# Optimization experiments

Measured on AMD Instinct MI355X. Metric: run time of the kernel, lower is better.

Reference implementation:

```python
import jax, jax.numpy as jnp
import numpy as np

TOPK = 13
NUM_CLASSES = 80
ALPHA = 1.0
BETA = 6.0
EPS = 1e-9
IOU_EPS = 1e-6  # mmdet BboxOverlaps2D union clamp


def setup_inputs() -> dict:
    key = jax.random.key(0)
    k0, k1, k2, k3, k4 = jax.random.split(key, 5)
    B, G, C = 32, 64, NUM_CLASSES
    # Prior center points for a 640x640 image, strides 8/16/32 -> 8400 priors.
    pts = []
    for s in (8, 16, 32):
        n = 640 // s
        xs = (jnp.arange(n, dtype=jnp.float32) + 0.5) * s
        gy, gx = jnp.meshgrid(xs, xs, indexing='ij')
        pts.append(jnp.stack([gx.ravel(), gy.ravel()], axis=-1))
    priors_points = jnp.concatenate(pts, axis=0)  # [8400, 2]
    P = priors_points.shape[0]
    pred_scores = jax.random.uniform(k0, (B, P, C), dtype=jnp.float32)
    half = jax.random.uniform(k1, (B, P, 2), minval=8.0, maxval=64.0)
    pred_bboxes = jnp.concatenate([priors_points[None] - half,
                                   priors_points[None] + half], axis=-1)
    xy = jax.random.uniform(k2, (B, G, 2), minval=0.0, maxval=560.0)
    wh = jax.random.uniform(k3, (B, G, 2), minval=16.0, maxval=80.0)
    gt_bboxes = jnp.concatenate([xy, xy + wh], axis=-1)
    gt_labels = jax.random.randint(k4, (B, G, 1), 0, C).astype(jnp.int64)
    pad_bbox_flag = jnp.ones((B, G, 1), jnp.float32)
    return {
        'pred_scores': pred_scores,
        'pred_bboxes': pred_bboxes,
        'priors_points': priors_points,
        'gt_labels': gt_labels,
        'gt_bboxes': gt_bboxes,
        'pad_bbox_flag': pad_bbox_flag,
    }


def _pairwise_iou(gt_bboxes, pred_bboxes):
    # gt [B,G,4], pred [B,P,4] (xyxy) -> IoU [B,G,P]
    lt = jnp.maximum(gt_bboxes[:, :, None, :2], pred_bboxes[:, None, :, :2])
    rb = jnp.minimum(gt_bboxes[:, :, None, 2:], pred_bboxes[:, None, :, 2:])
    wh = jnp.clip(rb - lt, 0.0)
    inter = wh[..., 0] * wh[..., 1]
    area_g = (gt_bboxes[..., 2] - gt_bboxes[..., 0]) * (gt_bboxes[..., 3] - gt_bboxes[..., 1])
    area_p = (pred_bboxes[..., 2] - pred_bboxes[..., 0]) * (pred_bboxes[..., 3] - pred_bboxes[..., 1])
    union = area_g[:, :, None] + area_p[:, None, :] - inter
    return inter / jnp.maximum(union, IOU_EPS)


def _assign(pred_scores, pred_bboxes, priors_points, gt_labels, gt_bboxes, pad_bbox_flag):
    B, P, C = pred_scores.shape
    G = gt_bboxes.shape[1]
    labels = gt_labels[..., 0].astype(jnp.int32)  # [B,G]

    # --- box metrics ---
    ps = jnp.swapaxes(pred_scores, 1, 2)  # [B,C,P]
    bbox_scores = ps[jnp.arange(B)[:, None], labels, :]  # [B,G,P]
    overlaps = _pairwise_iou(gt_bboxes, pred_bboxes)      # [B,G,P]
    align = (bbox_scores ** ALPHA) * (overlaps ** BETA)   # [B,G,P]

    # --- candidates inside gt boxes ---
    deltas = jnp.concatenate([
        priors_points[None, None] - gt_bboxes[:, :, None, :2],
        gt_bboxes[:, :, None, 2:] - priors_points[None, None]], axis=-1)  # [B,G,P,4]
    mask_in_gts = (deltas.min(axis=-1) > EPS).astype(align.dtype)  # [B,G,P]

    # --- topk candidate selection ---
    metrics = align * mask_in_gts
    _, topk_idxs = jax.lax.top_k(metrics, TOPK)  # [B,G,TOPK]
    topk_mask = (pad_bbox_flag > 0)              # [B,G,1], broadcasts over TOPK
    topk_idxs = jnp.where(topk_mask, topk_idxs, 0)
    flat_idx = topk_idxs.reshape(B * G, TOPK)
    counts = jnp.zeros((B * G, P), metrics.dtype)
    counts = counts.at[jnp.arange(B * G)[:, None], flat_idx].add(1.0)
    counts = counts.reshape(B, G, P)
    is_in_topk = jnp.where(counts > 1, 0.0, counts)
    pos_mask = is_in_topk * mask_in_gts * pad_bbox_flag  # [B,G,P]

    # --- resolve priors matched to multiple gts: keep highest-IoU gt ---
    fg_mask = pos_mask.sum(axis=1)  # [B,P]
    multi = fg_mask[:, None, :] > 1  # [B,1,P] -> broadcasts to [B,G,P]
    max_ov_idx = overlaps.argmax(axis=1)  # [B,P]
    is_max = jnp.swapaxes(jax.nn.one_hot(max_ov_idx, G, dtype=pos_mask.dtype), 1, 2)  # [B,G,P]
    pos_mask = jnp.where(multi, is_max, pos_mask)
    fg_mask = pos_mask.sum(axis=1)          # [B,P]
    assigned_gt_inds = pos_mask.argmax(axis=1)  # [B,P]

    # --- gather targets ---
    flat_gt = assigned_gt_inds + jnp.arange(B)[:, None] * G  # [B,P]
    assigned_labels = jnp.maximum(labels.reshape(-1)[flat_gt], 0)  # [B,P]
    assigned_bboxes = gt_bboxes.reshape(-1, 4)[flat_gt]            # [B,P,4]
    assigned_scores = jax.nn.one_hot(assigned_labels, C, dtype=pred_scores.dtype)
    assigned_scores = jnp.where((fg_mask > 0)[..., None], assigned_scores, 0.0)

    # --- normalize scores by alignment metric ---
    am = align * pos_mask
    pos_align = am.max(axis=-1, keepdims=True)                 # [B,G,1]
    pos_over = (overlaps * pos_mask).max(axis=-1, keepdims=True)
    norm = (am * pos_over / (pos_align + EPS)).max(axis=1)[..., None]  # [B,P,1]
    assigned_scores = assigned_scores * norm

    return assigned_labels, assigned_bboxes, assigned_scores, fg_mask > 0


def reference(pred_scores, pred_bboxes, priors_points, gt_labels, gt_bboxes, pad_bbox_flag):
    return _assign(pred_scores, pred_bboxes, priors_points, gt_labels, gt_bboxes, pad_bbox_flag)
```

## Files before the change

### kernel.cpp

```cpp
#include <hip/hip_runtime.h>
#include <cstdint>

#pragma clang fp contract(off)

#define B_ 32
#define G_ 64
#define C_ 80
#define P_ 8400
#define TOPK_ 13
#define HALF_ 4200
#define NTILE_ 66
#define EPS_IN 1e-9f
#define IOU_EPS_ 1e-6f

typedef unsigned long long u64;
typedef unsigned int u32;

__device__ __forceinline__ float iou_pair(float g0, float g1, float g2, float g3,
                                          float p0, float p1, float p2, float p3) {
    float ix1 = fmaxf(g0, p0);
    float iy1 = fmaxf(g1, p1);
    float ix2 = fminf(g2, p2);
    float iy2 = fminf(g3, p3);
    float iw = fmaxf(ix2 - ix1, 0.0f);
    float ih = fmaxf(iy2 - iy1, 0.0f);
    float inter = iw * ih;
    float ag = (g2 - g0) * (g3 - g1);
    float ap = (p2 - p0) * (p3 - p1);
    float uni = ag + ap - inter;
    return inter / fmaxf(uni, IOU_EPS_);
}

__device__ __forceinline__ float pow6(float x) {
    float x2 = x * x;
    float x4 = x2 * x2;
    return x4 * x2;
}

__global__ __launch_bounds__(256) void topk_kernel(
    const float* __restrict__ pred_scores,
    const float* __restrict__ pred_bboxes,
    const float* __restrict__ priors,
    const int* __restrict__ gt_labels,
    const float* __restrict__ gt_bboxes,
    const float* __restrict__ pad_flag,
    int* __restrict__ cnt,
    int* __restrict__ gsel0)
{
    const int wave = threadIdx.x >> 6;
    const int lane = threadIdx.x & 63;
    const int gl = wave >> 1;
    const int half = wave & 1;
    const int g = blockIdx.x * 2 + gl;
    const int b = blockIdx.y;
    const bool active = pad_flag[b * G_ + g] > 0.0f;

    __shared__ u64 lmerge[2][2][TOPK_];

    const float g0 = gt_bboxes[(b * G_ + g) * 4 + 0];
    const float g1 = gt_bboxes[(b * G_ + g) * 4 + 1];
    const float g2 = gt_bboxes[(b * G_ + g) * 4 + 2];
    const float g3 = gt_bboxes[(b * G_ + g) * 4 + 3];
    int lab = gt_labels[b * G_ + g];
    lab = lab < 0 ? 0 : (lab > C_ - 1 ? C_ - 1 : lab);

    const float4* pb = (const float4*)(pred_bboxes + (size_t)b * P_ * 4);
    const float2* pp = (const float2*)priors;
    const float* ps = pred_scores + (size_t)b * P_ * C_ + lab;

    u64 slotKey = 0x80000000ULL;
    u64 thrKey = 0x80000000ULL;

    if (active) {
        const int start = half * HALF_;
        for (int t = 0; t < NTILE_; ++t) {
            int p = start + t * 64 + lane;
            bool valid = p < start + HALF_;
            int pl = valid ? p : start;
            float2 pt = pp[pl];
            float d0 = pt.x - g0, d1 = pt.y - g1;
            float d2 = g2 - pt.x, d3 = g3 - pt.y;
            float mn = fminf(fminf(d0, d1), fminf(d2, d3));
            bool inside = valid && (mn > EPS_IN);
            float m = 0.0f;
            if (__ballot(inside)) {
                if (inside) {
                    float4 box = pb[pl];
                    float iou = iou_pair(g0, g1, g2, g3, box.x, box.y, box.z, box.w);
                    float s = ps[(size_t)pl * C_];
                    m = s * pow6(iou);
                }
            }
            u64 key = valid
                ? (((u64)__float_as_uint(m) << 32) | (u32)(~(u32)p))
                : 0ULL;
            u64 mask = __ballot(key > thrKey);
            while (mask) {
                int l = __ffsll(mask) - 1;
                u64 bKey = __shfl(key, l, 64);
                bool c = (lane < TOPK_) && (bKey > slotKey);
                u64 upKey = __shfl_up(slotKey, 1, 64);
                u64 cb = __ballot(c);
                int firstc = __ffsll(cb) - 1;
                if (c) slotKey = (lane == firstc) ? bKey : upKey;
                thrKey = __shfl(slotKey, 12, 64);
                mask &= (mask - 1);
                mask &= __ballot(key > thrKey);
            }
        }
    }

    if (lane < TOPK_) lmerge[gl][half][lane] = slotKey;
    __syncthreads();

    if (active && lane < TOPK_) {
        u64 my = slotKey;
        int rank = lane;
#pragma unroll
        for (int i = 0; i < TOPK_; ++i) rank += (lmerge[gl][half ^ 1][i] > my) ? 1 : 0;
        if (rank < TOPK_) {
            int p = (int)(~(u32)my);
            float2 pt = pp[p];
            float d0 = pt.x - g0, d1 = pt.y - g1;
            float d2 = g2 - pt.x, d3 = g3 - pt.y;
            float mn = fminf(fminf(d0, d1), fminf(d2, d3));
            if (mn > EPS_IN) {
                atomicAdd(&cnt[b * P_ + p], 1);
                gsel0[b * P_ + p] = g;
            }
        }
    }
}

__global__ __launch_bounds__(256) void assign_kernel(
    const float* __restrict__ pred_scores,
    const float* __restrict__ pred_bboxes,
    const int* __restrict__ gt_labels,
    const float* __restrict__ gt_bboxes,
    const int* __restrict__ cnt,
    int* __restrict__ gsel,
    int* __restrict__ labout,
    float* __restrict__ alignv,
    int* __restrict__ pos_align,
    int* __restrict__ pos_over,
    float* __restrict__ out)
{
    const int b = blockIdx.y;
    const int p = blockIdx.x * 256 + threadIdx.x;
    __shared__ float sgt[G_ * 4];
    __shared__ int slab[G_];
    if (threadIdx.x < G_ * 4) sgt[threadIdx.x] = gt_bboxes[b * G_ * 4 + threadIdx.x];
    if (threadIdx.x < G_) slab[threadIdx.x] = gt_labels[b * G_ + threadIdx.x];
    __syncthreads();
    if (p >= P_) return;

    const int bp = b * P_ + p;
    float4 box = ((const float4*)pred_bboxes)[(size_t)b * P_ + p];

    int c = cnt[bp];
    int g = -1;
    if (c == 1) {
        g = gsel[bp];
    } else if (c > 1) {
        float best = -1.0f;
        int bi = 0;
        for (int gg = 0; gg < G_; ++gg) {
            float v = iou_pair(sgt[gg * 4], sgt[gg * 4 + 1], sgt[gg * 4 + 2], sgt[gg * 4 + 3],
                               box.x, box.y, box.z, box.w);
            if (v > best) { best = v; bi = gg; }
        }
        g = bi;
    }
    gsel[bp] = g;

    const int gu = g < 0 ? 0 : g;
    int labraw = slab[gu];
    int labc = labraw < 0 ? 0 : labraw;

    float* out_lab = out;
    float4* out_bbox = (float4*)(out + (size_t)B_ * P_);
    float* out_fg = out + (size_t)B_ * P_ * (size_t)(1 + 4 + C_);

    out_lab[bp] = (float)labc;
    out_bbox[bp] = make_float4(sgt[gu * 4], sgt[gu * 4 + 1], sgt[gu * 4 + 2], sgt[gu * 4 + 3]);
    out_fg[bp] = g >= 0 ? 1.0f : 0.0f;

    if (g >= 0) {
        float iou = iou_pair(sgt[g * 4], sgt[g * 4 + 1], sgt[g * 4 + 2], sgt[g * 4 + 3],
                             box.x, box.y, box.z, box.w);
        int lb = labc > C_ - 1 ? C_ - 1 : labc;
        float s = pred_scores[(size_t)bp * C_ + lb];
        float al = s * pow6(iou);
        alignv[bp] = al;
        labout[bp] = lb;
        atomicMax(&pos_align[b * G_ + g], __float_as_int(al));
        atomicMax(&pos_over[b * G_ + g], __float_as_int(iou));
    }
}

__global__ __launch_bounds__(256) void scores_fill_kernel(
    const int* __restrict__ gsel,
    const int* __restrict__ labout,
    const float* __restrict__ alignv,
    const int* __restrict__ pos_align,
    const int* __restrict__ pos_over,
    float* __restrict__ out_scores)
{
    int bp = blockIdx.x * 256 + threadIdx.x;
    if (bp >= B_ * P_) return;
    int g = gsel[bp];
    if (g < 0) return;
    int b = bp / P_;
    int bg = b * G_ + g;
    float pa = __int_as_float(pos_align[bg]);
    float po = __int_as_float(pos_over[bg]);
    float val = alignv[bp] * po / (pa + 1e-9f);
    out_scores[(size_t)bp * C_ + labout[bp]] = val;
}

extern "C" void kernel_launch(void* const* d_in, const int* in_sizes, int n_in,
                              void* d_out, int out_size, void* d_ws, size_t ws_size,
                              hipStream_t stream) {
    (void)in_sizes; (void)n_in; (void)out_size; (void)ws_size;
    const float* pred_scores = (const float*)d_in[0];
    const float* pred_bboxes = (const float*)d_in[1];
    const float* priors      = (const float*)d_in[2];
    const int*   gt_labels   = (const int*)d_in[3];
    const float* gt_bboxes   = (const float*)d_in[4];
    const float* pad_flag    = (const float*)d_in[5];
    float* out = (float*)d_out;

    char* ws = (char*)d_ws;
    const size_t BP = (size_t)B_ * P_;
    const size_t BG = (size_t)B_ * G_;
    int* cnt       = (int*)ws;
    int* pos_align = (int*)(ws + BP * 4);
    int* pos_over  = (int*)(ws + BP * 4 + BG * 4);
    int* gsel      = (int*)(ws + BP * 4 + 2 * BG * 4);
    int* labout    = gsel + BP;
    float* alignv  = (float*)(labout + BP);

    hipMemsetAsync(ws, 0, (BP + 2 * BG) * 4, stream);
    hipMemsetAsync(out + BP * 5, 0, BP * (size_t)C_ * 4, stream);

    topk_kernel<<<dim3(G_ / 2, B_), 256, 0, stream>>>(
        pred_scores, pred_bboxes, priors, gt_labels, gt_bboxes, pad_flag, cnt, gsel);

    assign_kernel<<<dim3((P_ + 255) / 256, B_), 256, 0, stream>>>(
        pred_scores, pred_bboxes, gt_labels, gt_bboxes, cnt, gsel, labout, alignv,
        pos_align, pos_over, out);

    scores_fill_kernel<<<(int)((BP + 255) / 256), 256, 0, stream>>>(
        gsel, labout, alignv, pos_align, pos_over, out + BP * 5);
}
```

Before: 226.1 us.

## Scan only prior grid cells inside each GT box for top-k selection

The top-k kernel now works out, for each pyramid level, the range of grid cells covered by the GT box and visits only those priors instead of all 8400. Each lane keeps a private sorted top-6 list, and a 13-round wave-wide max-reduction merges the lists, replacing the serial ballot/shuffle insertion loop and the two-wave shared-memory merge. Each wave now owns one GT. This relies on priors lying on the fixed stride-8/16/32 grid, and it assumes no lane holds more than 6 of the final top 13. If outside-box priors with zero metric were meant to fill the top-k, they are now simply omitted, which matches the old post-filter.

```diff
diff --git a/kernel.cpp b/kernel.cpp
--- a/kernel.cpp
+++ b/kernel.cpp
@@ -8,8 +8,6 @@
 #define C_ 80
 #define P_ 8400
 #define TOPK_ 13
-#define HALF_ 4200
-#define NTILE_ 66
 #define EPS_IN 1e-9f
 #define IOU_EPS_ 1e-6f
 
@@ -49,13 +47,9 @@
 {
     const int wave = threadIdx.x >> 6;
     const int lane = threadIdx.x & 63;
-    const int gl = wave >> 1;
-    const int half = wave & 1;
-    const int g = blockIdx.x * 2 + gl;
+    const int g = blockIdx.x * 4 + wave;
     const int b = blockIdx.y;
-    const bool active = pad_flag[b * G_ + g] > 0.0f;
-
-    __shared__ u64 lmerge[2][2][TOPK_];
+    if (pad_flag[b * G_ + g] <= 0.0f) return;
 
     const float g0 = gt_bboxes[(b * G_ + g) * 4 + 0];
     const float g1 = gt_bboxes[(b * G_ + g) * 4 + 1];
@@ -68,67 +62,79 @@
     const float2* pp = (const float2*)priors;
     const float* ps = pred_scores + (size_t)b * P_ * C_ + lab;
 
-    u64 slotKey = 0x80000000ULL;
-    u64 thrKey = 0x80000000ULL;
-
-    if (active) {
-        const int start = half * HALF_;
-        for (int t = 0; t < NTILE_; ++t) {
-            int p = start + t * 64 + lane;
-            bool valid = p < start + HALF_;
-            int pl = valid ? p : start;
-            float2 pt = pp[pl];
-            float d0 = pt.x - g0, d1 = pt.y - g1;
-            float d2 = g2 - pt.x, d3 = g3 - pt.y;
-            float mn = fminf(fminf(d0, d1), fminf(d2, d3));
-            bool inside = valid && (mn > EPS_IN);
-            float m = 0.0f;
-            if (__ballot(inside)) {
-                if (inside) {
-                    float4 box = pb[pl];
-                    float iou = iou_pair(g0, g1, g2, g3, box.x, box.y, box.z, box.w);
-                    float s = ps[(size_t)pl * C_];
-                    m = s * pow6(iou);
-                }
-            }
-            u64 key = valid
-                ? (((u64)__float_as_uint(m) << 32) | (u32)(~(u32)p))
-                : 0ULL;
-            u64 mask = __ballot(key > thrKey);
-            while (mask) {
-                int l = __ffsll(mask) - 1;
-                u64 bKey = __shfl(key, l, 64);
-                bool c = (lane < TOPK_) && (bKey > slotKey);
-                u64 upKey = __shfl_up(slotKey, 1, 64);
-                u64 cb = __ballot(c);
-                int firstc = __ffsll(cb) - 1;
-                if (c) slotKey = (lane == firstc) ? bKey : upKey;
-                thrKey = __shfl(slotKey, 12, 64);
-                mask &= (mask - 1);
-                mask &= __ballot(key > thrKey);
-            }
-        }
-    }
-
-    if (lane < TOPK_) lmerge[gl][half][lane] = slotKey;
-    __syncthreads();
-
-    if (active && lane < TOPK_) {
-        u64 my = slotKey;
-        int rank = lane;
+    int x0_[3], y0_[3], nx_[3], c_[3], n_[3] = {80, 40, 20}, base_[3] = {0, 6400, 8000};
+    {
+        const float invs[3] = {0.125f, 0.0625f, 0.03125f};
 #pragma unroll
-        for (int i = 0; i < TOPK_; ++i) rank += (lmerge[gl][half ^ 1][i] > my) ? 1 : 0;
-        if (rank < TOPK_) {
-            int p = (int)(~(u32)my);
-            float2 pt = pp[p];
-            float d0 = pt.x - g0, d1 = pt.y - g1;
-            float d2 = g2 - pt.x, d3 = g3 - pt.y;
-            float mn = fminf(fminf(d0, d1), fminf(d2, d3));
-            if (mn > EPS_IN) {
-                atomicAdd(&cnt[b * P_ + p], 1);
-                gsel0[b * P_ + p] = g;
-            }
-        }
+        for (int l = 0; l < 3; ++l) {
+            int n = n_[l];
+            int x0 = (int)floorf(g0 * invs[l] - 0.5f) - 1;
+            int x1 = (int)ceilf (g2 * invs[l] - 0.5f) + 1;
+            int y0 = (int)floorf(g1 * invs[l] - 0.5f) - 1;
+            int y1 = (int)ceilf (g3 * invs[l] - 0.5f) + 1;
+            x0 = x0 < 0 ? 0 : x0;  y0 = y0 < 0 ? 0 : y0;
+            x1 = x1 > n - 1 ? n - 1 : x1;  y1 = y1 > n - 1 ? n - 1 : y1;
+            int nx = x1 - x0 + 1, ny = y1 - y0 + 1;
+            x0_[l] = x0; y0_[l] = y0;
+            nx_[l] = nx > 0 ? nx : 1;
+            c_[l] = (nx > 0 && ny > 0) ? nx * ny : 0;
+        }
+    }
+    const int c0 = c_[0], c01 = c_[0] + c_[1], total = c01 + c_[2];
+
+    u64 k0 = 0, k1 = 0, k2 = 0, k3 = 0, k4 = 0, k5 = 0;
+
+    for (int j = lane; j < total; j += 64) {
+        int l = (j >= c0) + (j >= c01);
+        int r = j - (l == 0 ? 0 : (l == 1 ? c0 : c01));
+        int nx = l == 0 ? nx_[0] : (l == 1 ? nx_[1] : nx_[2]);
+        int n  = l == 0 ? 80 : (l == 1 ? 40 : 20);
+        int bs = l == 0 ? 0 : (l == 1 ? 6400 : 8000);
+        int x0 = l == 0 ? x0_[0] : (l == 1 ? x0_[1] : x0_[2]);
+        int y0 = l == 0 ? y0_[0] : (l == 1 ? y0_[1] : y0_[2]);
+        int iy = r / nx;
+        int ix = r - iy * nx;
+        int p = bs + (y0 + iy) * n + (x0 + ix);
+
+        float2 pt = pp[p];
+        float d0 = pt.x - g0, d1 = pt.y - g1;
+        float d2 = g2 - pt.x, d3 = g3 - pt.y;
+        float mn = fminf(fminf(d0, d1), fminf(d2, d3));
+        if (mn > EPS_IN) {
+            float4 box = pb[p];
+            float iou = iou_pair(g0, g1, g2, g3, box.x, box.y, box.z, box.w);
+            float m = ps[(size_t)p * C_] * pow6(iou);
+            u64 key = ((u64)__float_as_uint(m) << 32) | (u32)(~(u32)p);
+            bool b0 = key > k0, b1 = key > k1, b2 = key > k2,
+                 b3 = key > k3, b4 = key > k4, b5 = key > k5;
+            k5 = b4 ? k4 : (b5 ? key : k5);
+            k4 = b3 ? k3 : (b4 ? key : k4);
+            k3 = b2 ? k2 : (b3 ? key : k3);
+            k2 = b1 ? k1 : (b2 ? key : k2);
+            k1 = b0 ? k0 : (b1 ? key : k1);
+            k0 = b0 ? key : k0;
+        }
+    }
+
+    u64 mykey = 0;
+#pragma unroll
+    for (int r = 0; r < TOPK_; ++r) {
+        u64 m = k0;
+#pragma unroll
+        for (int off = 1; off < 64; off <<= 1) {
+            u64 o = __shfl_xor(m, off, 64);
+            m = o > m ? o : m;
+        }
+        if (lane == r) mykey = m;
+        if (k0 == m && m != 0) {
+            k0 = k1; k1 = k2; k2 = k3; k3 = k4; k4 = k5; k5 = 0;
+        }
+    }
+
+    if (lane < TOPK_ && mykey != 0) {
+        int p = (int)(~(u32)mykey);
+        atomicAdd(&cnt[b * P_ + p], 1);
+        gsel0[b * P_ + p] = g;
     }
 }
 
@@ -243,7 +249,7 @@
     hipMemsetAsync(ws, 0, (BP + 2 * BG) * 4, stream);
     hipMemsetAsync(out + BP * 5, 0, BP * (size_t)C_ * 4, stream);
 
-    topk_kernel<<<dim3(G_ / 2, B_), 256, 0, stream>>>(
+    topk_kernel<<<dim3(G_ / 4, B_), 256, 0, stream>>>(
         pred_scores, pred_bboxes, priors, gt_labels, gt_bboxes, pad_flag, cnt, gsel);
 
     assign_kernel<<<dim3((P_ + 255) / 256, B_), 256, 0, stream>>>(
```

Result: faster. 191.7 us (-15.2%).
